# Kernel optimization log

Measured on AMD Instinct MI355X. Metric: run time of the kernel, lower is better.

## Reference

```python
import jax, jax.numpy as jnp
import numpy as np

EPS = 1e-12  # torch spectral_norm default eps


def _l2norm(v):
    return v / (jnp.linalg.norm(v) + EPS)


def _spectral_norm_2d(w, u):
    # one power iteration (torch default n_power_iterations=1), u/v detached
    v = _l2norm(w.T @ u)
    u_new = _l2norm(w @ v)
    u_new = jax.lax.stop_gradient(u_new)
    v = jax.lax.stop_gradient(v)
    sigma = u_new @ (w @ v)
    return w / sigma


def _spectral_norm_1d(b):
    # torch._SpectralNorm for ndim==1: F.normalize(weight, dim=0)
    return b / (jnp.linalg.norm(b) + EPS)


def setup_inputs() -> dict:
    key = jax.random.key(0)
    ks = jax.random.split(key, 8)
    T, B, I, H = 4096, 32, 256, 256
    s_i = 1.0 / np.sqrt(H)  # nn.RNN init: U(-1/sqrt(H), 1/sqrt(H))
    return {
        "x": jax.random.normal(ks[0], (T, B, I), jnp.float32),
        "state": jax.random.normal(ks[1], (1, B, H), jnp.float32),
        "w_ih": jax.random.uniform(ks[2], (H, I), jnp.float32, -s_i, s_i),
        "w_hh": jax.random.uniform(ks[3], (H, H), jnp.float32, -s_i, s_i),
        "b_ih": jax.random.uniform(ks[4], (H,), jnp.float32, -s_i, s_i),
        "b_hh": jax.random.uniform(ks[5], (H,), jnp.float32, -s_i, s_i),
        "u_ih": jax.random.normal(ks[6], (H,), jnp.float32),  # power-iteration buffer
        "u_hh": jax.random.normal(ks[7], (H,), jnp.float32),
    }


def reference(x, state, w_ih, w_hh, b_ih, b_hh, u_ih, u_hh):
    # spectral-norm parametrization of all RNN weights
    w_ih_sn = _spectral_norm_2d(w_ih, _l2norm(u_ih))
    w_hh_sn = _spectral_norm_2d(w_hh, _l2norm(u_hh))
    b_sn = _spectral_norm_1d(b_ih) + _spectral_norm_1d(b_hh)

    # input projection batched over all timesteps: [T,B,H]
    pre = jnp.einsum("tbi,hi->tbh", x, w_ih_sn) + b_sn

    def step(h, p):
        h_new = jnp.tanh(p + h @ w_hh_sn.T)
        return h_new, h_new

    h_last, out = jax.lax.scan(step, state[0], pre)
    return out, h_last[None]
```

## Files before the change

### kernel.cpp

```cpp
#include <hip/hip_runtime.h>
#include <hip/hip_bf16.h>
#include <math.h>

#define EPSF 1e-12f
#define H 256
#define TSTEPS 4096
#define BATCH 32
#define TB (TSTEPS*BATCH)
#define BH (BATCH*H)

typedef _Float16 h2 __attribute__((ext_vector_type(2)));

#if defined(__has_builtin)
#if __has_builtin(__builtin_amdgcn_fdot2)
#define FDOT2(a, b, c) __builtin_amdgcn_fdot2((a), (b), (c), false)
#endif
#endif
#ifndef FDOT2
#define FDOT2(a, b, c) fmaf((float)(a).y, (float)(b).y, fmaf((float)(a).x, (float)(b).x, (c)))
#endif

#define BC(u) __builtin_bit_cast(h2, (u))

__device__ __forceinline__ void bar_nodrain() {
  __builtin_amdgcn_sched_barrier(0);
  asm volatile("s_waitcnt lgkmcnt(0)" ::: "memory");
  __builtin_amdgcn_s_barrier();
  __builtin_amdgcn_sched_barrier(0);
}

__device__ __forceinline__ float block_sum256(float v, float* red) {
  #pragma unroll
  for (int o = 32; o > 0; o >>= 1) v += __shfl_down(v, o, 64);
  __syncthreads();
  if ((threadIdx.x & 63) == 0) red[threadIdx.x >> 6] = v;
  __syncthreads();
  return red[0] + red[1] + red[2] + red[3];
}

__global__ __launch_bounds__(256) void k_prep(
    const float* __restrict__ w_ih, const float* __restrict__ w_hh,
    const float* __restrict__ b_ih, const float* __restrict__ b_hh,
    const float* __restrict__ u_ih, const float* __restrict__ u_hh,
    float* __restrict__ wsc) {
  __shared__ float red[4];
  __shared__ float ubuf[H];
  __shared__ float vbuf[H];
  const int tid = threadIdx.x;

  float inv_sig[2];
  const float* Ws[2] = {w_ih, w_hh};
  const float* Us[2] = {u_ih, u_hh};
  #pragma unroll 1
  for (int m = 0; m < 2; m++) {
    const float* W = Ws[m];
    float uv = Us[m][tid];
    float nu = sqrtf(block_sum256(uv * uv, red));
    ubuf[tid] = uv / (nu + EPSF);
    __syncthreads();
    float vt = 0.f;
    for (int h = 0; h < H; h++) vt = fmaf(W[h * H + tid], ubuf[h], vt);
    float nv = sqrtf(block_sum256(vt * vt, red));
    vbuf[tid] = vt / (nv + EPSF);
    __syncthreads();
    float wv = 0.f;
    const float* wr = W + (size_t)tid * H;
    for (int i = 0; i < H; i++) wv = fmaf(wr[i], vbuf[i], wv);
    float n2 = block_sum256(wv * wv, red);
    float sigma = n2 / (sqrtf(n2) + EPSF);
    inv_sig[m] = 1.f / sigma;
  }
  float bi = b_ih[tid], bh = b_hh[tid];
  float nbi = sqrtf(block_sum256(bi * bi, red));
  float nbh = sqrtf(block_sum256(bh * bh, red));
  wsc[tid] = bi / (nbi + EPSF) + bh / (nbh + EPSF);
  if (tid == 0) { wsc[H] = inv_sig[0]; wsc[H + 1] = inv_sig[1]; }
}

__global__ __launch_bounds__(256) void k_pre(
    const float* __restrict__ x, const float* __restrict__ w_ih,
    const float* __restrict__ wsc, float* __restrict__ pre) {
  __shared__ float xs[32 * 256];
  const int tid = threadIdx.x;
  const size_t m0 = (size_t)blockIdx.x * 32;

  const float4* xp = (const float4*)(x + m0 * H);
  float4* xsv = (float4*)xs;
  #pragma unroll
  for (int j = 0; j < 8; j++) xsv[j * 256 + tid] = xp[j * 256 + tid];
  __syncthreads();

  float acc[32];
  #pragma unroll
  for (int m = 0; m < 32; m++) acc[m] = 0.f;

  const float* wrow = w_ih + (size_t)tid * H;
  #pragma unroll 1
  for (int kb = 0; kb < 256; kb += 8) {
    float4 wa = *(const float4*)(wrow + kb);
    float4 wb = *(const float4*)(wrow + kb + 4);
    #pragma unroll
    for (int m = 0; m < 32; m++) {
      const float* xr = xs + m * 256 + kb;
      float4 xa = *(const float4*)xr;
      float4 xb = *(const float4*)(xr + 4);
      float a = acc[m];
      a = fmaf(xa.x, wa.x, a); a = fmaf(xa.y, wa.y, a);
      a = fmaf(xa.z, wa.z, a); a = fmaf(xa.w, wa.w, a);
      a = fmaf(xb.x, wb.x, a); a = fmaf(xb.y, wb.y, a);
      a = fmaf(xb.z, wb.z, a); a = fmaf(xb.w, wb.w, a);
      acc[m] = a;
    }
  }
  const float inv_s = wsc[H];
  const float bsn = wsc[tid];
  #pragma unroll
  for (int m = 0; m < 32; m++)
    pre[(m0 + m) * H + tid] = fmaf(acc[m], inv_s, bsn);
}

__global__ __launch_bounds__(512, 1) void k_scan(
    const float* __restrict__ state, const float* __restrict__ w_hh,
    const float* __restrict__ wsc, float* __restrict__ out) {
  __shared__ __align__(16) _Float16 hbuf[2][H];
  __shared__ __align__(16) float part[8][H];
  const int tid = threadIdx.x;
  const int cg = tid >> 6;
  const int q  = tid & 63;
  const int r0 = q << 2;
  const int b = blockIdx.x;
  const float inv_s = wsc[H + 1];

  h2 wreg[4][16];
  #pragma unroll
  for (int i = 0; i < 4; i++) {
    const float* wr = w_hh + (size_t)(r0 + i) * H + (cg << 5);
    #pragma unroll
    for (int c = 0; c < 16; c++) {
      float2 wv = *(const float2*)(wr + 2 * c);
      wreg[i][c] = h2{(_Float16)(wv.x * inv_s), (_Float16)(wv.y * inv_s)};
    }
  }

  if (tid < H) hbuf[0][tid] = (_Float16)state[b * H + tid];
  float* outb = out + (size_t)b * H + tid;
  float pre0 = 0.f, pre1 = 0.f;
  if (tid < H) { pre0 = outb[0]; pre1 = outb[BH]; }
  bar_nodrain();

  float hn = 0.f;
  #pragma unroll 1
  for (int t = 0; t < TSTEPS; t++) {
    float pre2 = 0.f;
    if (tid < H) {
      int tn = (t + 2 <= TSTEPS) ? (t + 2) : TSTEPS;
      pre2 = outb[(size_t)tn * BH];
    }

    const uint4* hb = (const uint4*)(hbuf[t & 1] + (cg << 5));
    uint4 q0 = hb[0], q1 = hb[1], q2 = hb[2], q3 = hb[3];

    float acc[4];
    #pragma unroll
    for (int i = 0; i < 4; i++) {
      float a = 0.f;
      a = FDOT2(wreg[i][ 0], BC(q0.x), a);
      a = FDOT2(wreg[i][ 1], BC(q0.y), a);
      a = FDOT2(wreg[i][ 2], BC(q0.z), a);
      a = FDOT2(wreg[i][ 3], BC(q0.w), a);
      a = FDOT2(wreg[i][ 4], BC(q1.x), a);
      a = FDOT2(wreg[i][ 5], BC(q1.y), a);
      a = FDOT2(wreg[i][ 6], BC(q1.z), a);
      a = FDOT2(wreg[i][ 7], BC(q1.w), a);
      a = FDOT2(wreg[i][ 8], BC(q2.x), a);
      a = FDOT2(wreg[i][ 9], BC(q2.y), a);
      a = FDOT2(wreg[i][10], BC(q2.z), a);
      a = FDOT2(wreg[i][11], BC(q2.w), a);
      a = FDOT2(wreg[i][12], BC(q3.x), a);
      a = FDOT2(wreg[i][13], BC(q3.y), a);
      a = FDOT2(wreg[i][14], BC(q3.z), a);
      a = FDOT2(wreg[i][15], BC(q3.w), a);
      acc[i] = a;
    }
    *(float4*)&part[cg][r0] = make_float4(acc[0], acc[1], acc[2], acc[3]);
    bar_nodrain();

    if (tid < H) {
      float s = pre0;
      #pragma unroll
      for (int g = 0; g < 8; g++) s += part[g][tid];
      float sc = fminf(fmaxf(s, -15.f), 15.f);
      float e = __expf(2.f * sc);
      hn = __fdividef(e - 1.f, e + 1.f);
      outb[(size_t)t * BH] = hn;
      hbuf[(t + 1) & 1][tid] = (_Float16)hn;
    }
    bar_nodrain();
    pre0 = pre1; pre1 = pre2;
  }
  if (tid < H) out[(size_t)TSTEPS * BH + b * H + tid] = hn;
}

extern "C" void kernel_launch(void* const* d_in, const int* in_sizes, int n_in,
                              void* d_out, int out_size, void* d_ws, size_t ws_size,
                              hipStream_t stream) {
  const float* x     = (const float*)d_in[0];
  const float* state = (const float*)d_in[1];
  const float* w_ih  = (const float*)d_in[2];
  const float* w_hh  = (const float*)d_in[3];
  const float* b_ih  = (const float*)d_in[4];
  const float* b_hh  = (const float*)d_in[5];
  const float* u_ih  = (const float*)d_in[6];
  const float* u_hh  = (const float*)d_in[7];
  float* out = (float*)d_out;
  float* wsc = (float*)d_ws;

  k_prep<<<1, 256, 0, stream>>>(w_ih, w_hh, b_ih, b_hh, u_ih, u_hh, wsc);
  k_pre<<<TB / 32, 256, 0, stream>>>(x, w_ih, wsc, out);
  k_scan<<<BATCH, 512, 0, stream>>>(state, w_hh, wsc, out);
}
```

Baseline: 2.736 ms.

## Reduce recurrent matvec partials with DPP lane swaps instead of shared memory

Each wave of the scan kernel now owns 32 output rows. A lane holds an 8x16 weight tile and computes 8 partial dot products, which are combined inside the wave by a butterfly of DPP row/half mirrors and quad swaps. This removes the shared-memory partial array and one of the two block barriers per timestep, so each step needs only one barrier after writing h. The h buffer gets an XOR swizzle to avoid LDS bank conflicts. The cost is more cross-lane ALU work and select instructions, plus redundant tanh computed on all lanes.

New measurement: 2.728 ms. No clear change (-0.3%).

```diff
diff --git a/kernel.cpp b/kernel.cpp
--- a/kernel.cpp
+++ b/kernel.cpp
@@ -21,6 +21,13 @@
 #endif
 
 #define BC(u) __builtin_bit_cast(h2, (u))
+
+#define DPPF(x, ctrl) __builtin_bit_cast(float, __builtin_amdgcn_update_dpp( \
+    0, __builtin_bit_cast(int, (x)), (ctrl), 0xf, 0xf, true))
+#define DPP_QUAD_XOR1 0xB1
+#define DPP_QUAD_XOR2 0x4E
+#define DPP_HALF_MIRROR 0x141
+#define DPP_ROW_MIRROR  0x140
 
 __device__ __forceinline__ void bar_nodrain() {
   __builtin_amdgcn_sched_barrier(0);
@@ -119,86 +126,102 @@
     pre[(m0 + m) * H + tid] = fmaf(acc[m], inv_s, bsn);
 }
 
+__device__ __forceinline__ int swz(int a) { return a ^ (((a >> 8) & 1) << 6); }
+
 __global__ __launch_bounds__(512, 1) void k_scan(
     const float* __restrict__ state, const float* __restrict__ w_hh,
     const float* __restrict__ wsc, float* __restrict__ out) {
   __shared__ __align__(16) _Float16 hbuf[2][H];
-  __shared__ __align__(16) float part[8][H];
   const int tid = threadIdx.x;
-  const int cg = tid >> 6;
-  const int q  = tid & 63;
-  const int r0 = q << 2;
+  const int cg   = tid >> 6;
+  const int q    = tid & 63;
+  const int rgrp = q >> 4;
+  const int kseg = q & 15;
+  const int jrow = 4 * ((q >> 3) & 1) + 2 * ((q >> 2) & 1) + ((q >> 1) & 1);
+  const int myrow = (cg << 5) + (rgrp << 3) + jrow;
   const int b = blockIdx.x;
   const float inv_s = wsc[H + 1];
-
-  h2 wreg[4][16];
-  #pragma unroll
-  for (int i = 0; i < 4; i++) {
-    const float* wr = w_hh + (size_t)(r0 + i) * H + (cg << 5);
+  const bool hb3 = (q >> 3) & 1, hb2 = (q >> 2) & 1, hb1 = (q >> 1) & 1;
+
+  h2 wreg[8][8];
+  #pragma unroll
+  for (int i = 0; i < 8; i++) {
+    const float* wr = w_hh + (size_t)((cg << 5) + (rgrp << 3) + i) * H + (kseg << 4);
     #pragma unroll
-    for (int c = 0; c < 16; c++) {
+    for (int c = 0; c < 8; c++) {
       float2 wv = *(const float2*)(wr + 2 * c);
       wreg[i][c] = h2{(_Float16)(wv.x * inv_s), (_Float16)(wv.y * inv_s)};
     }
   }
 
-  if (tid < H) hbuf[0][tid] = (_Float16)state[b * H + tid];
-  float* outb = out + (size_t)b * H + tid;
-  float pre0 = 0.f, pre1 = 0.f;
-  if (tid < H) { pre0 = outb[0]; pre1 = outb[BH]; }
+  const int a0s = swz(kseg << 5);
+  const int a1s = swz((kseg << 5) + 16);
+  const int woff = swz(myrow * 2);
+
+  if (tid < H)
+    *(_Float16*)((char*)&hbuf[0][0] + swz(tid * 2)) = (_Float16)state[b * H + tid];
+
+  const float* pbase = out + (size_t)b * H + myrow;
+  float pre0 = pbase[0], pre1 = pbase[BH];
   bar_nodrain();
 
   float hn = 0.f;
   #pragma unroll 1
   for (int t = 0; t < TSTEPS; t++) {
-    float pre2 = 0.f;
-    if (tid < H) {
-      int tn = (t + 2 <= TSTEPS) ? (t + 2) : TSTEPS;
-      pre2 = outb[(size_t)tn * BH];
-    }
-
-    const uint4* hb = (const uint4*)(hbuf[t & 1] + (cg << 5));
-    uint4 q0 = hb[0], q1 = hb[1], q2 = hb[2], q3 = hb[3];
-
-    float acc[4];
+    int tn = (t + 2 <= TSTEPS) ? (t + 2) : TSTEPS;
+    float pre2 = pbase[(size_t)tn * BH];
+
+    const char* hb = (const char*)&hbuf[t & 1][0];
+    uint4 q0 = *(const uint4*)(hb + a0s);
+    uint4 q1 = *(const uint4*)(hb + a1s);
+
+    float acc[8];
     #pragma unroll
-    for (int i = 0; i < 4; i++) {
+    for (int i = 0; i < 8; i++) {
       float a = 0.f;
-      a = FDOT2(wreg[i][ 0], BC(q0.x), a);
-      a = FDOT2(wreg[i][ 1], BC(q0.y), a);
-      a = FDOT2(wreg[i][ 2], BC(q0.z), a);
-      a = FDOT2(wreg[i][ 3], BC(q0.w), a);
-      a = FDOT2(wreg[i][ 4], BC(q1.x), a);
-      a = FDOT2(wreg[i][ 5], BC(q1.y), a);
-      a = FDOT2(wreg[i][ 6], BC(q1.z), a);
-      a = FDOT2(wreg[i][ 7], BC(q1.w), a);
-      a = FDOT2(wreg[i][ 8], BC(q2.x), a);
-      a = FDOT2(wreg[i][ 9], BC(q2.y), a);
-      a = FDOT2(wreg[i][10], BC(q2.z), a);
-      a = FDOT2(wreg[i][11], BC(q2.w), a);
-      a = FDOT2(wreg[i][12], BC(q3.x), a);
-      a = FDOT2(wreg[i][13], BC(q3.y), a);
-      a = FDOT2(wreg[i][14], BC(q3.z), a);
-      a = FDOT2(wreg[i][15], BC(q3.w), a);
+      a = FDOT2(wreg[i][0], BC(q0.x), a);
+      a = FDOT2(wreg[i][1], BC(q0.y), a);
+      a = FDOT2(wreg[i][2], BC(q0.z), a);
+      a = FDOT2(wreg[i][3], BC(q0.w), a);
+      a = FDOT2(wreg[i][4], BC(q1.x), a);
+      a = FDOT2(wreg[i][5], BC(q1.y), a);
+      a = FDOT2(wreg[i][6], BC(q1.z), a);
+      a = FDOT2(wreg[i][7], BC(q1.w), a);
       acc[i] = a;
     }
-    *(float4*)&part[cg][r0] = make_float4(acc[0], acc[1], acc[2], acc[3]);
-    bar_nodrain();
-
-    if (tid < H) {
-      float s = pre0;
-      #pragma unroll
-      for (int g = 0; g < 8; g++) s += part[g][tid];
-      float sc = fminf(fmaxf(s, -15.f), 15.f);
-      float e = __expf(2.f * sc);
-      hn = __fdividef(e - 1.f, e + 1.f);
-      outb[(size_t)t * BH] = hn;
-      hbuf[(t + 1) & 1][tid] = (_Float16)hn;
+
+    float v0, v1, v2, v3;
+    { float k0 = hb3 ? acc[4] : acc[0], s0 = hb3 ? acc[0] : acc[4];
+      float k1 = hb3 ? acc[5] : acc[1], s1 = hb3 ? acc[1] : acc[5];
+      float k2 = hb3 ? acc[6] : acc[2], s2 = hb3 ? acc[2] : acc[6];
+      float k3 = hb3 ? acc[7] : acc[3], s3 = hb3 ? acc[3] : acc[7];
+      v0 = k0 + DPPF(s0, DPP_ROW_MIRROR);
+      v1 = k1 + DPPF(s1, DPP_ROW_MIRROR);
+      v2 = k2 + DPPF(s2, DPP_ROW_MIRROR);
+      v3 = k3 + DPPF(s3, DPP_ROW_MIRROR); }
+    float u0, u1;
+    { float k0 = hb2 ? v2 : v0, s0 = hb2 ? v0 : v2;
+      float k1 = hb2 ? v3 : v1, s1 = hb2 ? v1 : v3;
+      u0 = k0 + DPPF(s0, DPP_HALF_MIRROR);
+      u1 = k1 + DPPF(s1, DPP_HALF_MIRROR); }
+    float ssum;
+    { float k0 = hb1 ? u1 : u0, s0 = hb1 ? u0 : u1;
+      ssum = k0 + DPPF(s0, DPP_QUAD_XOR2); }
+    ssum += DPPF(ssum, DPP_QUAD_XOR1);
+
+    float s = ssum + pre0;
+    float sc = fminf(fmaxf(s, -15.f), 15.f);
+    float e = __expf(2.f * sc);
+    hn = __fdividef(e - 1.f, e + 1.f);
+
+    if (!(q & 1)) {
+      *(_Float16*)((char*)&hbuf[(t + 1) & 1][0] + woff) = (_Float16)hn;
+      out[(size_t)t * BH + b * H + myrow] = hn;
     }
     bar_nodrain();
     pre0 = pre1; pre1 = pre2;
   }
-  if (tid < H) out[(size_t)TSTEPS * BH + b * H + tid] = hn;
+  if (!(q & 1)) out[(size_t)TSTEPS * BH + b * H + myrow] = hn;
 }
 
 extern "C" void kernel_launch(void* const* d_in, const int* in_sizes, int n_in,
```
